# Kernel optimization log

Measured on AMD Instinct MI355X. Metric: run time of the kernel, lower is better.

The kernel has to match this reference:

```python
import jax, jax.numpy as jnp
import numpy as np

T, B, I, H = 512, 64, 1024, 1024
SIGMA = 0.01

def setup_inputs() -> dict:
    key = jax.random.key(0)
    k1, k2, k3 = jax.random.split(key, 3)
    X = jax.random.normal(k1, (T, B, I), dtype=jnp.float32)
    W_xh = jax.random.normal(k2, (I, H), dtype=jnp.float32) * SIGMA
    W_hh = jax.random.normal(k3, (H, H), dtype=jnp.float32) * SIGMA
    b_h = jnp.zeros((H,), dtype=jnp.float32)
    return {"X": X, "W_xh": W_xh, "W_hh": W_hh, "b_h": b_h}

def reference(X, W_xh, W_hh, b_h):
    # Precompute input projection for all timesteps in one big GEMM: [T,B,I]@[I,H]
    Xp = jnp.einsum('tbi,ih->tbh', X, W_xh) + b_h
    state0 = jnp.zeros((X.shape[1], W_hh.shape[0]), dtype=X.dtype)

    def step(state, xp_t):
        new_state = jnp.tanh(xp_t + state @ W_hh)
        return new_state, new_state

    final_state, outputs = jax.lax.scan(step, state0, Xp)
    return outputs, final_state
```

## Files before the change

kernel.cpp:

```cpp
#include <hip/hip_runtime.h>
#include <hip/hip_bf16.h>
#include <stdint.h>

typedef short bf16x8 __attribute__((ext_vector_type(8)));
typedef float f32x4  __attribute__((ext_vector_type(4)));
typedef unsigned int u32x4 __attribute__((ext_vector_type(4)));

static __device__ __forceinline__ unsigned short bf16_rne(float f) {
    unsigned u = __builtin_bit_cast(unsigned, f);
    unsigned r = u + 0x7fffu + ((u >> 16) & 1u);
    return (unsigned short)(r >> 16);
}
static __device__ __forceinline__ float bf16tof(unsigned short h) {
    unsigned u = ((unsigned)h) << 16;
    return __builtin_bit_cast(float, u);
}

__global__ __launch_bounds__(256) void k_transpose(const float* __restrict__ W,
                                                   unsigned short* __restrict__ Wt) {
    __shared__ float tile[64][65];
    int bx = blockIdx.x & 15, by = blockIdx.x >> 4;
    int n0 = bx * 64, k0 = by * 64;
    int tx = threadIdx.x & 63, ty = threadIdx.x >> 6;
#pragma unroll
    for (int p = 0; p < 16; ++p) {
        int r = p * 4 + ty;
        tile[r][tx] = W[(size_t)(k0 + r) * 1024 + n0 + tx];
    }
    __syncthreads();
#pragma unroll
    for (int p = 0; p < 16; ++p) {
        int r = p * 4 + ty;
        Wt[(size_t)(n0 + r) * 1024 + k0 + tx] = bf16_rne(tile[tx][r]);
    }
}

#define LDA 80

__global__ __launch_bounds__(256) void k_xpgemm(const float* __restrict__ X,
                                                const unsigned short* __restrict__ Wt,
                                                const float* __restrict__ bh,
                                                unsigned short* __restrict__ Xp) {
    __shared__ __align__(16) unsigned char ldsA[128 * LDA];
    __shared__ __align__(16) unsigned char ldsB[128 * LDA];
    int p = blockIdx.x;
    int lo = (p & 7) * 256 + (p >> 3);
    int mt = lo >> 3, nt = lo & 7;
    int m0 = mt * 128, n0 = nt * 128;
    int tid = threadIdx.x;
    int lane = tid & 63, wid = tid >> 6;
    int wr = wid >> 1, wc = wid & 1;
    int mw = wr * 64, nw = wc * 64;
    int l15 = lane & 15, kg = lane >> 4;

    f32x4 acc[4][4] = {};
    int arow = tid >> 3, as = tid & 7;
    int brow = tid >> 2, bs = tid & 3;

    for (int kt = 0; kt < 32; ++kt) {
#pragma unroll
        for (int pp = 0; pp < 4; ++pp) {
            int r = pp * 32 + arow;
            const float4 v = *(const float4*)(X + (size_t)(m0 + r) * 1024 + kt * 32 + as * 4);
            unsigned lo32 = ((unsigned)bf16_rne(v.y) << 16) | bf16_rne(v.x);
            unsigned hi32 = ((unsigned)bf16_rne(v.w) << 16) | bf16_rne(v.z);
            *(uint2*)(ldsA + r * LDA + as * 8) = make_uint2(lo32, hi32);
        }
#pragma unroll
        for (int pp = 0; pp < 2; ++pp) {
            int r = pp * 64 + brow;
            uint4 v = *(const uint4*)(Wt + (size_t)(n0 + r) * 1024 + kt * 32 + bs * 8);
            *(uint4*)(ldsB + r * LDA + bs * 16) = v;
        }
        __syncthreads();
        bf16x8 af[4];
#pragma unroll
        for (int i = 0; i < 4; ++i)
            af[i] = *(const bf16x8*)(ldsA + (mw + 16 * i + l15) * LDA + kg * 16);
#pragma unroll
        for (int j = 0; j < 4; ++j) {
            bf16x8 bfj = *(const bf16x8*)(ldsB + (nw + 16 * j + l15) * LDA + kg * 16);
#pragma unroll
            for (int i = 0; i < 4; ++i)
                acc[i][j] = __builtin_amdgcn_mfma_f32_16x16x32_bf16(af[i], bfj, acc[i][j], 0, 0, 0);
        }
        __syncthreads();
    }
#pragma unroll
    for (int j = 0; j < 4; ++j) {
        int col = n0 + nw + 16 * j + l15;
        float bias = bh[col];
#pragma unroll
        for (int i = 0; i < 4; ++i) {
            int rb = m0 + mw + 16 * i + kg * 4;
#pragma unroll
            for (int r = 0; r < 4; ++r)
                Xp[(size_t)(rb + r) * 1024 + col] = bf16_rne(acc[i][j][r] + bias);
        }
    }
}

#define SB0 __builtin_amdgcn_sched_barrier(0)
#define WAITV0 asm volatile("s_waitcnt vmcnt(0)" ::: "memory")
#define WAITV4 asm volatile("s_waitcnt vmcnt(4)" ::: "memory")

#define LDT(d, a, O) asm volatile("global_load_dwordx4 %0, %1, off offset:" #O " sc1" : "=v"(d) : "v"(a) : "memory")
#define LDU(d, a, O) asm volatile("global_load_ushort %0, %1, off offset:" #O : "=v"(d) : "v"(a) : "memory")
#define STS(a, v, O) asm volatile("global_store_short %0, %1, off offset:" #O " sc1" :: "v"(a), "v"(v) : "memory")
#define STD(a, v, O) asm volatile("global_store_dword %0, %1, off offset:" #O " sc1" :: "v"(a), "v"(v) : "memory")

#define ISSUE32H(B, A) do { \
    LDT(B[0],(A),0);     LDT(B[1],(A),64);    LDT(B[2],(A),128);   LDT(B[3],(A),192);   \
    LDT(B[4],(A),256);   LDT(B[5],(A),320);   LDT(B[6],(A),384);   LDT(B[7],(A),448);   \
    LDT(B[8],(A),512);   LDT(B[9],(A),576);   LDT(B[10],(A),640);  LDT(B[11],(A),704);  \
    LDT(B[12],(A),768);  LDT(B[13],(A),832);  LDT(B[14],(A),896);  LDT(B[15],(A),960);  \
    LDT(B[16],(A),1024); LDT(B[17],(A),1088); LDT(B[18],(A),1152); LDT(B[19],(A),1216); \
    LDT(B[20],(A),1280); LDT(B[21],(A),1344); LDT(B[22],(A),1408); LDT(B[23],(A),1472); \
    LDT(B[24],(A),1536); LDT(B[25],(A),1600); LDT(B[26],(A),1664); LDT(B[27],(A),1728); \
    LDT(B[28],(A),1792); LDT(B[29],(A),1856); LDT(B[30],(A),1920); LDT(B[31],(A),1984); } while (0)

__global__ __launch_bounds__(64, 1) void k_scan(const float* __restrict__ Whh,
                                                const unsigned short* __restrict__ Xp,
                                                unsigned short* __restrict__ hbuf,
                                                unsigned int* flags,
                                                float* __restrict__ out) {
    const int wid = blockIdx.x;
    const int rt = wid >> 6, ct = wid & 63;
    const int j0 = ct * 16, b0 = rt * 16;
    const int lane = threadIdx.x;
    const int l15 = lane & 15, kg = lane >> 4;
    const int jj = j0 + l15;
    const int rbase = b0 + kg * 4;

    bf16x8 w[32];
#pragma unroll
    for (int i = 0; i < 32; ++i) {
#pragma unroll
        for (int e = 0; e < 8; ++e)
            w[i][e] = (short)bf16_rne(Whh[(size_t)(i * 32 + kg * 8 + e) * 1024 + jj]);
    }

    const uint64_t fp = (uint64_t)(flags + rt * 64 + lane);
    const uint64_t myflag = (uint64_t)(flags + wid);
    const uint64_t hrd = (uint64_t)hbuf + (uint64_t)(b0 + l15) * 2048 + kg * 16;
    const uint64_t hwr = (uint64_t)hbuf + (uint64_t)rbase * 2048 + (uint64_t)jj * 2;
    const uint64_t xb  = (uint64_t)Xp + (uint64_t)(rbase * 1024 + jj) * 2;

    u32x4 hr[32];
    unsigned xr[4];
    float hv[4];

    for (int t = 0; t < 512; ++t) {
        if (t > 0) {
            unsigned tt = (unsigned)t;
            for (;;) {
                unsigned f;
                asm volatile("global_load_dword %0, %1, off sc1\n\t"
                             "s_waitcnt vmcnt(0)"
                             : "=v"(f) : "v"(fp) : "memory");
                if (__all((int)(f >= tt))) break;
            }
        }
        SB0;

        const uint64_t hp = hrd + ((uint64_t)(t & 1) << 17);
        ISSUE32H(hr, hp);
        const uint64_t xa = xb + (uint64_t)t * 131072;
        LDU(xr[0], xa, 0); LDU(xr[1], xa, 2048);
        LDU(xr[2], xa + 4096, 0); LDU(xr[3], xa + 4096, 2048);

        WAITV4; SB0;

        f32x4 a0 = {0.f, 0.f, 0.f, 0.f}, a1 = {0.f, 0.f, 0.f, 0.f};
        f32x4 a2 = {0.f, 0.f, 0.f, 0.f}, a3 = {0.f, 0.f, 0.f, 0.f};
#pragma unroll
        for (int ks = 0; ks < 8; ++ks) {
            a0 = __builtin_amdgcn_mfma_f32_16x16x32_bf16(
                __builtin_bit_cast(bf16x8, hr[4 * ks + 0]), w[4 * ks + 0], a0, 0, 0, 0);
            a1 = __builtin_amdgcn_mfma_f32_16x16x32_bf16(
                __builtin_bit_cast(bf16x8, hr[4 * ks + 1]), w[4 * ks + 1], a1, 0, 0, 0);
            a2 = __builtin_amdgcn_mfma_f32_16x16x32_bf16(
                __builtin_bit_cast(bf16x8, hr[4 * ks + 2]), w[4 * ks + 2], a2, 0, 0, 0);
            a3 = __builtin_amdgcn_mfma_f32_16x16x32_bf16(
                __builtin_bit_cast(bf16x8, hr[4 * ks + 3]), w[4 * ks + 3], a3, 0, 0, 0);
        }
        f32x4 acc = (a0 + a1) + (a2 + a3);

        WAITV0; SB0;

        unsigned hb[4];
#pragma unroll
        for (int r = 0; r < 4; ++r) {
            float z = acc[r] + bf16tof((unsigned short)xr[r]);
            z = fminf(fmaxf(z, -15.f), 15.f);
            float e = __expf(2.f * z);
            float v = (e - 1.f) / (e + 1.f);
            hv[r] = v;
            hb[r] = (unsigned)bf16_rne(v);
        }

        if (t < 511) {
            const uint64_t hn = hwr + ((uint64_t)((t + 1) & 1) << 17);
            STS(hn, hb[0], 0); STS(hn + 2048, hb[1], 0);
            STS(hn + 4096, hb[2], 0); STS(hn + 6144, hb[3], 0);
            WAITV0;
            if (lane == 0)
                STD(myflag, (unsigned)(t + 1), 0);
        }

#pragma unroll
        for (int r = 0; r < 4; ++r)
            out[(size_t)(t * 64 + rbase + r) * 1024 + jj] = hv[r];
    }
#pragma unroll
    for (int r = 0; r < 4; ++r)
        out[(size_t)33554432 + (size_t)(rbase + r) * 1024 + jj] = hv[r];
}

extern "C" void kernel_launch(void* const* d_in, const int* in_sizes, int n_in,
                              void* d_out, int out_size, void* d_ws, size_t ws_size,
                              hipStream_t stream) {
    const float* X   = (const float*)d_in[0];
    const float* Wxh = (const float*)d_in[1];
    const float* Whh = (const float*)d_in[2];
    const float* bh  = (const float*)d_in[3];
    float* out = (float*)d_out;
    unsigned char* ws = (unsigned char*)d_ws;

    unsigned short* Wt    = (unsigned short*)(ws);
    unsigned short* Xp    = (unsigned short*)(ws + 2097152);
    unsigned short* hbuf  = (unsigned short*)(ws + 69206016);
    unsigned int*   flags = (unsigned int*)(ws + 69468160);

    hipMemsetAsync(ws + 69206016, 0, 263168, stream);
    hipLaunchKernelGGL(k_transpose, dim3(256), dim3(256), 0, stream, Wxh, Wt);
    hipLaunchKernelGGL(k_xpgemm, dim3(2048), dim3(256), 0, stream, X, Wt, bh, Xp);
    hipLaunchKernelGGL(k_scan, dim3(256), dim3(64), 0, stream, Whh, Xp, hbuf, flags, out);
}
```

Baseline: 2.582 ms.

## Group scan waves into 8-wave blocks sharing hidden state via LDS

Restructures the recurrent scan from 256 single-wave blocks into 32 blocks of 8 waves. Each block loads the 16-row hidden-state slice once cooperatively into LDS, and the waves read their MFMA operands from LDS. Cross-block sync now polls 8 flags per block instead of 64 per wave, with __syncthreads inside each block. This cuts redundant global hidden-state reads and flag polling but adds block barriers and an LDS staging step to every timestep.

```diff
diff --git a/kernel.cpp b/kernel.cpp
--- a/kernel.cpp
+++ b/kernel.cpp
@@ -102,34 +102,24 @@
 
 #define SB0 __builtin_amdgcn_sched_barrier(0)
 #define WAITV0 asm volatile("s_waitcnt vmcnt(0)" ::: "memory")
-#define WAITV4 asm volatile("s_waitcnt vmcnt(4)" ::: "memory")
-
 #define LDT(d, a, O) asm volatile("global_load_dwordx4 %0, %1, off offset:" #O " sc1" : "=v"(d) : "v"(a) : "memory")
-#define LDU(d, a, O) asm volatile("global_load_ushort %0, %1, off offset:" #O : "=v"(d) : "v"(a) : "memory")
 #define STS(a, v, O) asm volatile("global_store_short %0, %1, off offset:" #O " sc1" :: "v"(a), "v"(v) : "memory")
 #define STD(a, v, O) asm volatile("global_store_dword %0, %1, off offset:" #O " sc1" :: "v"(a), "v"(v) : "memory")
 
-#define ISSUE32H(B, A) do { \
-    LDT(B[0],(A),0);     LDT(B[1],(A),64);    LDT(B[2],(A),128);   LDT(B[3],(A),192);   \
-    LDT(B[4],(A),256);   LDT(B[5],(A),320);   LDT(B[6],(A),384);   LDT(B[7],(A),448);   \
-    LDT(B[8],(A),512);   LDT(B[9],(A),576);   LDT(B[10],(A),640);  LDT(B[11],(A),704);  \
-    LDT(B[12],(A),768);  LDT(B[13],(A),832);  LDT(B[14],(A),896);  LDT(B[15],(A),960);  \
-    LDT(B[16],(A),1024); LDT(B[17],(A),1088); LDT(B[18],(A),1152); LDT(B[19],(A),1216); \
-    LDT(B[20],(A),1280); LDT(B[21],(A),1344); LDT(B[22],(A),1408); LDT(B[23],(A),1472); \
-    LDT(B[24],(A),1536); LDT(B[25],(A),1600); LDT(B[26],(A),1664); LDT(B[27],(A),1728); \
-    LDT(B[28],(A),1792); LDT(B[29],(A),1856); LDT(B[30],(A),1920); LDT(B[31],(A),1984); } while (0)
-
-__global__ __launch_bounds__(64, 1) void k_scan(const float* __restrict__ Whh,
-                                                const unsigned short* __restrict__ Xp,
-                                                unsigned short* __restrict__ hbuf,
-                                                unsigned int* flags,
-                                                float* __restrict__ out) {
-    const int wid = blockIdx.x;
-    const int rt = wid >> 6, ct = wid & 63;
-    const int j0 = ct * 16, b0 = rt * 16;
-    const int lane = threadIdx.x;
+__global__ __launch_bounds__(512) void k_scan(const float* __restrict__ Whh,
+                                              const unsigned short* __restrict__ Xp,
+                                              unsigned short* __restrict__ hbuf,
+                                              unsigned int* flags,
+                                              float* __restrict__ out) {
+    __shared__ __align__(16) unsigned char lds[32 * 16 * 80];
+
+    const int bid = blockIdx.x;
+    const int rt = bid >> 3, wct = bid & 7;
+    const int b0 = rt * 16;
+    const int tid = threadIdx.x;
+    const int lane = tid & 63, wid = tid >> 6;
     const int l15 = lane & 15, kg = lane >> 4;
-    const int jj = j0 + l15;
+    const int jj = wct * 128 + wid * 16 + l15;
     const int rbase = b0 + kg * 4;
 
     bf16x8 w[32];
@@ -140,58 +130,64 @@
             w[i][e] = (short)bf16_rne(Whh[(size_t)(i * 32 + kg * 8 + e) * 1024 + jj]);
     }
 
-    const uint64_t fp = (uint64_t)(flags + rt * 64 + lane);
-    const uint64_t myflag = (uint64_t)(flags + wid);
-    const uint64_t hrd = (uint64_t)hbuf + (uint64_t)(b0 + l15) * 2048 + kg * 16;
+    const uint64_t fpoll  = (uint64_t)(flags + rt * 8 + (lane & 7));
+    const uint64_t myflag = (uint64_t)(flags + bid);
+
+    const int crow = tid >> 5;
+    const int cclb = (tid & 31) * 64;
+    const uint64_t crd = (uint64_t)hbuf + (uint64_t)(b0 + crow) * 2048 + cclb;
+    unsigned char* ldsw = lds + (tid & 31) * 1280 + crow * 80;
+
     const uint64_t hwr = (uint64_t)hbuf + (uint64_t)rbase * 2048 + (uint64_t)jj * 2;
-    const uint64_t xb  = (uint64_t)Xp + (uint64_t)(rbase * 1024 + jj) * 2;
-
-    u32x4 hr[32];
-    unsigned xr[4];
+    const unsigned short* xpb = Xp + (size_t)rbase * 1024 + jj;
+
     float hv[4];
 
     for (int t = 0; t < 512; ++t) {
-        if (t > 0) {
+        if (t > 0 && wid == 0) {
             unsigned tt = (unsigned)t;
             for (;;) {
                 unsigned f;
                 asm volatile("global_load_dword %0, %1, off sc1\n\t"
                              "s_waitcnt vmcnt(0)"
-                             : "=v"(f) : "v"(fp) : "memory");
+                             : "=v"(f) : "v"(fpoll) : "memory");
                 if (__all((int)(f >= tt))) break;
             }
         }
-        SB0;
-
-        const uint64_t hp = hrd + ((uint64_t)(t & 1) << 17);
-        ISSUE32H(hr, hp);
-        const uint64_t xa = xb + (uint64_t)t * 131072;
-        LDU(xr[0], xa, 0); LDU(xr[1], xa, 2048);
-        LDU(xr[2], xa + 4096, 0); LDU(xr[3], xa + 4096, 2048);
-
-        WAITV4; SB0;
+        __syncthreads();
+
+        u32x4 c0, c1, c2, c3;
+        const uint64_t ca = crd + ((uint64_t)(t & 1) << 17);
+        LDT(c0, ca, 0); LDT(c1, ca, 16); LDT(c2, ca, 32); LDT(c3, ca, 48);
+        unsigned short xr[4];
+#pragma unroll
+        for (int r = 0; r < 4; ++r)
+            xr[r] = xpb[(size_t)t * 65536 + r * 1024];
+        WAITV0; SB0;
+        *(u32x4*)(ldsw)      = c0; *(u32x4*)(ldsw + 16) = c1;
+        *(u32x4*)(ldsw + 32) = c2; *(u32x4*)(ldsw + 48) = c3;
+        __syncthreads();
 
         f32x4 a0 = {0.f, 0.f, 0.f, 0.f}, a1 = {0.f, 0.f, 0.f, 0.f};
         f32x4 a2 = {0.f, 0.f, 0.f, 0.f}, a3 = {0.f, 0.f, 0.f, 0.f};
+        const unsigned char* lrd = lds + l15 * 80 + kg * 16;
 #pragma unroll
         for (int ks = 0; ks < 8; ++ks) {
             a0 = __builtin_amdgcn_mfma_f32_16x16x32_bf16(
-                __builtin_bit_cast(bf16x8, hr[4 * ks + 0]), w[4 * ks + 0], a0, 0, 0, 0);
+                *(const bf16x8*)(lrd + (4 * ks + 0) * 1280), w[4 * ks + 0], a0, 0, 0, 0);
             a1 = __builtin_amdgcn_mfma_f32_16x16x32_bf16(
-                __builtin_bit_cast(bf16x8, hr[4 * ks + 1]), w[4 * ks + 1], a1, 0, 0, 0);
+                *(const bf16x8*)(lrd + (4 * ks + 1) * 1280), w[4 * ks + 1], a1, 0, 0, 0);
             a2 = __builtin_amdgcn_mfma_f32_16x16x32_bf16(
-                __builtin_bit_cast(bf16x8, hr[4 * ks + 2]), w[4 * ks + 2], a2, 0, 0, 0);
+                *(const bf16x8*)(lrd + (4 * ks + 2) * 1280), w[4 * ks + 2], a2, 0, 0, 0);
             a3 = __builtin_amdgcn_mfma_f32_16x16x32_bf16(
-                __builtin_bit_cast(bf16x8, hr[4 * ks + 3]), w[4 * ks + 3], a3, 0, 0, 0);
+                *(const bf16x8*)(lrd + (4 * ks + 3) * 1280), w[4 * ks + 3], a3, 0, 0, 0);
         }
         f32x4 acc = (a0 + a1) + (a2 + a3);
 
-        WAITV0; SB0;
-
         unsigned hb[4];
 #pragma unroll
         for (int r = 0; r < 4; ++r) {
-            float z = acc[r] + bf16tof((unsigned short)xr[r]);
+            float z = acc[r] + bf16tof(xr[r]);
             z = fminf(fmaxf(z, -15.f), 15.f);
             float e = __expf(2.f * z);
             float v = (e - 1.f) / (e + 1.f);
@@ -204,9 +200,10 @@
             STS(hn, hb[0], 0); STS(hn + 2048, hb[1], 0);
             STS(hn + 4096, hb[2], 0); STS(hn + 6144, hb[3], 0);
             WAITV0;
-            if (lane == 0)
-                STD(myflag, (unsigned)(t + 1), 0);
-        }
+        }
+        __syncthreads();
+        if (t < 511 && tid == 0)
+            STD(myflag, (unsigned)(t + 1), 0);
 
 #pragma unroll
         for (int r = 0; r < 4; ++r)
@@ -235,5 +232,5 @@
     hipMemsetAsync(ws + 69206016, 0, 263168, stream);
     hipLaunchKernelGGL(k_transpose, dim3(256), dim3(256), 0, stream, Wxh, Wt);
     hipLaunchKernelGGL(k_xpgemm, dim3(2048), dim3(256), 0, stream, X, Wt, bh, Xp);
-    hipLaunchKernelGGL(k_scan, dim3(256), dim3(64), 0, stream, Whh, Xp, hbuf, flags, out);
-}
+    hipLaunchKernelGGL(k_scan, dim3(32), dim3(512), 0, stream, Whh, Xp, hbuf, flags, out);
+}
```

New measurement: 2.636 ms. +2.1%, slower.
